# Kernel tuning notes

Hardware: AMD Instinct MI355X
Metric: run time of the kernel (lower is better)

Reference implementation:

```python
import jax, jax.numpy as jnp
import numpy as np

N_EMBD = 768
FULL_SIZE = 16 * N_EMBD   # 12288
K = 4 * N_EMBD            # iter_size = 3072 (top-k)
B, T = 8, 1024


def setup_inputs() -> dict:
    key = jax.random.key(0)
    k0, k1, k2, k3, k4 = jax.random.split(key, 5)
    s = lambda fan_in: 1.0 / np.sqrt(fan_in)
    return {
        "x": jax.random.normal(k0, (B, T, N_EMBD), dtype=jnp.float32),
        "w1": jax.random.normal(k1, (N_EMBD // 16, N_EMBD), dtype=jnp.float32) * s(N_EMBD),
        "w2": jax.random.normal(k2, (FULL_SIZE, N_EMBD // 16), dtype=jnp.float32) * s(N_EMBD // 16),
        "w_mfc": jax.random.normal(k3, (FULL_SIZE, N_EMBD), dtype=jnp.float32) * s(N_EMBD),
        "w_proj": jax.random.normal(k4, (N_EMBD, FULL_SIZE), dtype=jnp.float32) * s(FULL_SIZE),
    }


def _topk_mask(ck, k):
    # softmax -> top-k indices -> hard 0/1 mask (scatter of constant 1.0)
    probs = jax.nn.softmax(ck, axis=-1)
    _, idx = jax.lax.top_k(probs, k)            # (B, k)
    b = jnp.arange(probs.shape[0])[:, None]
    return jnp.zeros_like(probs).at[b, idx].set(1.0)


def reference(x, w1, w2, w_mfc, w_proj):
    # control net on sequence-mean pooled features
    pooled = x.mean(axis=1)                                  # (B, D)
    ck = jax.nn.relu(pooled @ w1.T) @ w2.T                   # (B, F)
    mask = _topk_mask(ck, K)                                 # (B, F) hard 0/1
    # DynamicMaskedLinear: bmm(x, (W*mask)^T) == (x @ W^T) * mask (0/1 output mask)
    h = jnp.einsum('btd,fd->btf', x, w_mfc) * mask[:, None, :]
    h = jax.nn.relu(h)
    out = jnp.einsum('btf,ef->bte', h, w_proj)               # (B, T, D)
    return out
```

## Files before the change

kernel.cpp:

```cpp
#include <hip/hip_runtime.h>

#define N_EMBD 768
#define FULL   12288
#define KSEL   3072
#define BATCH  8
#define TLEN   1024
#define HID    48

typedef short bf16x8 __attribute__((ext_vector_type(8)));
typedef float f32x4 __attribute__((ext_vector_type(4)));
typedef unsigned short u16x4 __attribute__((ext_vector_type(4)));
typedef unsigned short u16x8 __attribute__((ext_vector_type(8)));

#define MFMA(a, b, c) __builtin_amdgcn_mfma_f32_16x16x32_bf16((a), (b), (c), 0, 0, 0)
#define GLDS(g, l) __builtin_amdgcn_global_load_lds( \
    (const __attribute__((address_space(1))) void*)(const void*)(g), \
    (__attribute__((address_space(3))) void*)(void*)(l), 16, 0, 0)

__device__ __forceinline__ unsigned short f2bf(float f) {
  unsigned u = __float_as_uint(f);
  u += 0x7fffu + ((u >> 16) & 1u);
  return (unsigned short)(u >> 16);
}
__device__ __forceinline__ float bf2f(unsigned short h) {
  return __uint_as_float(((unsigned)h) << 16);
}

__global__ void split_pool_x(const float* __restrict__ x, unsigned short* __restrict__ xh,
                             unsigned short* __restrict__ xl, float* __restrict__ partial) {
  const int s = blockIdx.x;
  const int b = blockIdx.y;
  const int d = blockIdx.z * 256 + threadIdx.x * 4;
  const float* base = x + ((size_t)(b * TLEN + s * 64)) * N_EMBD + d;
  float4 sum = {0.f, 0.f, 0.f, 0.f};
  for (int t = 0; t < 64; ++t) {
    const float4 v = *(const float4*)(base + (size_t)t * N_EMBD);
    sum.x += v.x; sum.y += v.y; sum.z += v.z; sum.w += v.w;
    u16x4 h, l;
    h.x = f2bf(v.x); l.x = f2bf(v.x - bf2f(h.x));
    h.y = f2bf(v.y); l.y = f2bf(v.y - bf2f(h.y));
    h.z = f2bf(v.z); l.z = f2bf(v.z - bf2f(h.z));
    h.w = f2bf(v.w); l.w = f2bf(v.w - bf2f(h.w));
    const size_t o = ((size_t)(b * TLEN + s * 64 + t)) * N_EMBD + d;
    *(u16x4*)(xh + o) = h;
    *(u16x4*)(xl + o) = l;
  }
  float* pp = partial + (b * 16 + s) * N_EMBD + d;
  pp[0] = sum.x; pp[1] = sum.y; pp[2] = sum.z; pp[3] = sum.w;
}

__global__ __launch_bounds__(256) void control1_kernel(
    const float* __restrict__ partial, const float* __restrict__ w1, float* __restrict__ hid) {
  __shared__ float w1s[HID][385];
  __shared__ float ps[N_EMBD];
  const int b = blockIdx.x;
  const int tid = threadIdx.x;
  for (int d = tid; d < N_EMBD; d += 256) {
    float sum = 0.f;
    #pragma unroll
    for (int s = 0; s < 16; ++s) sum += partial[(b * 16 + s) * N_EMBD + d];
    ps[d] = sum * (1.f / TLEN);
  }
  float acc = 0.f;
  #pragma unroll
  for (int half = 0; half < 2; ++half) {
    __syncthreads();
    for (int i = tid; i < HID * 384; i += 256) {
      const int r = i / 384, c = i % 384;
      w1s[r][c] = w1[r * N_EMBD + half * 384 + c];
    }
    __syncthreads();
    if (tid < HID) {
      const float* pr = ps + half * 384;
      #pragma unroll 8
      for (int d2 = 0; d2 < 384; ++d2) acc = fmaf(pr[d2], w1s[tid][d2], acc);
    }
  }
  if (tid < HID) hid[b * HID + tid] = fmaxf(acc, 0.f);
}

__global__ void control2_kernel(const float* __restrict__ hid, const float* __restrict__ w2,
                                float* __restrict__ ck) {
  const int b = blockIdx.y;
  const int f = blockIdx.x * 256 + threadIdx.x;
  __shared__ float hid_s[HID];
  if (threadIdx.x < HID) hid_s[threadIdx.x] = hid[b * HID + threadIdx.x];
  __syncthreads();
  const float* wr = w2 + (size_t)f * HID;
  float acc = 0.f;
  #pragma unroll
  for (int j = 0; j < HID; ++j) acc = fmaf(hid_s[j], wr[j], acc);
  ck[b * FULL + f] = acc;
}

__global__ void topk_kernel(const float* __restrict__ ck, int* __restrict__ sel) {
  const int b = blockIdx.x;
  const int tid = threadIdx.x;
  const int lane = tid & 63, wv = tid >> 6;
  unsigned key[48];
  const int f_lo = tid * 48;
  #pragma unroll
  for (int i = 0; i < 48; ++i) {
    unsigned u = __float_as_uint(ck[b * FULL + f_lo + i]);
    key[i] = (u & 0x80000000u) ? ~u : (u | 0x80000000u);
  }
  __shared__ unsigned redw[4];
  __shared__ int sg[257], se[257];
  unsigned prefix = 0;
  int remaining = KSEL;
  for (int bit = 31; bit >= 0; --bit) {
    const unsigned want = prefix | (1u << bit);
    const unsigned shifted = want >> bit;
    int cnt = 0;
    #pragma unroll
    for (int i = 0; i < 48; ++i) cnt += ((key[i] >> bit) == shifted) ? 1 : 0;
    #pragma unroll
    for (int off = 1; off < 64; off <<= 1) cnt += __shfl_xor(cnt, off, 64);
    if (lane == 0) redw[wv] = (unsigned)cnt;
    __syncthreads();
    const int c = (int)(redw[0] + redw[1] + redw[2] + redw[3]);
    __syncthreads();
    if (c >= remaining) prefix = want;
    else remaining -= c;
  }
  const unsigned kth = prefix;
  int cg = 0, ce = 0;
  #pragma unroll
  for (int i = 0; i < 48; ++i) { cg += (key[i] > kth) ? 1 : 0; ce += (key[i] == kth) ? 1 : 0; }
  sg[tid] = cg; se[tid] = ce;
  __syncthreads();
  if (tid == 0) {
    int ag = 0, ae = 0;
    for (int i = 0; i < 256; ++i) {
      int tg = sg[i], te = se[i];
      sg[i] = ag; se[i] = ae;
      ag += tg; ae += te;
    }
    sg[256] = ag;
  }
  __syncthreads();
  const int ng = sg[256];
  int gpos = sg[tid], epos = se[tid];
  #pragma unroll
  for (int i = 0; i < 48; ++i) {
    const unsigned k = key[i];
    const int f = f_lo + i;
    if (k > kth) {
      sel[b * KSEL + (gpos++)] = f;
    } else if (k == kth) {
      const int p = ng + epos;
      if (p < KSEL) sel[b * KSEL + p] = f;
      ++epos;
    }
  }
}

__global__ void round_w_kernel(const float* __restrict__ src, unsigned short* __restrict__ dst, int n4) {
  const int idx = blockIdx.x * 256 + threadIdx.x;
  if (idx >= n4) return;
  const float4 v = ((const float4*)src)[idx];
  u16x4 h;
  h.x = f2bf(v.x); h.y = f2bf(v.y); h.z = f2bf(v.z); h.w = f2bf(v.w);
  ((u16x4*)dst)[idx] = h;
}

__global__ __launch_bounds__(256) void gather_wp_kernel(
    const float* __restrict__ wproj, const int* __restrict__ sel,
    unsigned short* __restrict__ wph) {
  __shared__ unsigned short row_s[FULL];
  const int e = blockIdx.x;
  const int tid = threadIdx.x;
  const float* wr = wproj + (size_t)e * FULL;
  #pragma unroll
  for (int i = 0; i < FULL / 4 / 256; ++i) {
    const int idx = tid + i * 256;
    const float4 v = ((const float4*)wr)[idx];
    u16x4 h;
    h.x = f2bf(v.x); h.y = f2bf(v.y); h.z = f2bf(v.z); h.w = f2bf(v.w);
    *(u16x4*)(row_s + idx * 4) = h;
  }
  __syncthreads();
  #pragma unroll
  for (int i = 0; i < 12; ++i) {
    const int idx = tid + i * 256;
    const int b = idx / 384, c = idx % 384;
    const int* sp = sel + b * KSEL + c * 8;
    const int4 s0 = ((const int4*)sp)[0];
    const int4 s1 = ((const int4*)sp)[1];
    u16x8 v;
    v[0] = row_s[s0.x]; v[1] = row_s[s0.y]; v[2] = row_s[s0.z]; v[3] = row_s[s0.w];
    v[4] = row_s[s1.x]; v[5] = row_s[s1.y]; v[6] = row_s[s1.z]; v[7] = row_s[s1.w];
    *(u16x8*)(wph + ((size_t)(b * N_EMBD + e)) * KSEL + c * 8) = v;
  }
}

__global__ __launch_bounds__(256) void gemm1_mfma(
    const unsigned short* __restrict__ xh, const unsigned short* __restrict__ xl,
    const unsigned short* __restrict__ wh, const int* __restrict__ sel,
    unsigned short* __restrict__ hh) {
  __shared__ __align__(16) char sm[49152];
  const int nx = TLEN / 128, ny = KSEL / 128;
  const int nwg = nx * ny * BATCH;
  int lin = blockIdx.x + nx * (blockIdx.y + ny * blockIdx.z);
  int swz = (lin & 7) * (nwg >> 3) + (lin >> 3);
  const int bx = swz % nx; int tmp = swz / nx;
  const int by = tmp % ny; const int b = tmp / ny;
  const int t0 = bx * 128, f0 = by * 128;

  const int tid = threadIdx.x;
  const int wv = tid >> 6, lane = tid & 63;
  const int srow = tid >> 2, sslot = tid & 3;
  const int wb = wv * 1024;

  const char* pxh = (const char*)xh;
  const char* pxl = (const char*)xl;
  const char* pwh = (const char*)wh;
  const size_t aoff  = ((size_t)(b * TLEN + t0 + srow)) * 1536 + sslot * 16;
  const size_t aoff2 = aoff + (size_t)64 * 1536;
  const int* selb = sel + b * KSEL;
  const size_t boff  = (size_t)selb[f0 + srow] * 1536 + sslot * 16;
  const size_t boff2 = (size_t)selb[f0 + srow + 64] * 1536 + sslot * 16;

  const int fr = lane & 15, kg = lane >> 4;
  const int fo = fr * 64 + kg * 16;
  const int m0 = (wv >> 1) * 64, n0 = (wv & 1) * 64;

  f32x4 acc[4][4];
  const f32x4 z4 = {0.f, 0.f, 0.f, 0.f};
  #pragma unroll
  for (int mi = 0; mi < 4; ++mi)
    #pragma unroll
    for (int ni = 0; ni < 4; ++ni) acc[mi][ni] = z4;

  auto stage = [&](int bo, int d) {
    GLDS(pxh + aoff  + d, sm + bo + 0     + wb);
    GLDS(pxh + aoff2 + d, sm + bo + 4096  + wb);
    GLDS(pxl + aoff  + d, sm + bo + 8192  + wb);
    GLDS(pxl + aoff2 + d, sm + bo + 12288 + wb);
    GLDS(pwh + boff  + d, sm + bo + 16384 + wb);
    GLDS(pwh + boff2 + d, sm + bo + 20480 + wb);
  };
  stage(0, 0);
  __syncthreads();
  const int NIT = N_EMBD * 2 / 64;
  for (int it = 0; it < NIT; ++it) {
    const int cur = (it & 1) ? 24576 : 0;
    if (it + 1 < NIT) stage(cur ^ 24576, (it + 1) * 64);
    bf16x8 ah[4], al[4], bh[4];
    #pragma unroll
    for (int i = 0; i < 4; ++i) {
      const int ra = (m0 + i * 16) * 64 + fo;
      const int rb = (n0 + i * 16) * 64 + fo;
      ah[i] = *(const bf16x8*)(sm + cur + 0     + ra);
      al[i] = *(const bf16x8*)(sm + cur + 8192  + ra);
      bh[i] = *(const bf16x8*)(sm + cur + 16384 + rb);
    }
    #pragma unroll
    for (int mi = 0; mi < 4; ++mi)
      #pragma unroll
      for (int ni = 0; ni < 4; ++ni) {
        acc[mi][ni] = MFMA(ah[mi], bh[ni], acc[mi][ni]);
        acc[mi][ni] = MFMA(al[mi], bh[ni], acc[mi][ni]);
      }
    __syncthreads();
  }
  unsigned short* lh = (unsigned short*)sm;
  const int rowg = lane >> 4, colc = lane & 15;
  #pragma unroll
  for (int mi = 0; mi < 4; ++mi)
    #pragma unroll
    for (int ni = 0; ni < 4; ++ni) {
      const int row = m0 + mi * 16 + rowg * 4;
      const int col = n0 + ni * 16 + colc;
      #pragma unroll
      for (int j = 0; j < 4; ++j)
        lh[(row + j) * 128 + col] = f2bf(fmaxf(acc[mi][ni][j], 0.f));
    }
  __syncthreads();
  const int orow = tid >> 4, oc = tid & 15;
  #pragma unroll
  for (int i2 = 0; i2 < 8; ++i2) {
    const int row = orow + i2 * 16;
    const u16x8 v = *(const u16x8*)&lh[row * 128 + oc * 8];
    *(u16x8*)(hh + ((size_t)(b * TLEN + t0 + row)) * KSEL + f0 + oc * 8) = v;
  }
}

__global__ __launch_bounds__(256) void gemm2_mfma(
    const unsigned short* __restrict__ hh, const unsigned short* __restrict__ wph,
    float* __restrict__ out) {
  __shared__ __align__(16) char sm[32768];
  const int lin = blockIdx.x;
  const int b = lin & 7;
  const int j = lin >> 3;
  const int bx = j & 7, by = j >> 3;
  const int t0 = bx * 128, e0 = by * 128;

  const int tid = threadIdx.x;
  const int wv = tid >> 6, lane = tid & 63;
  const int wb = wv * 1024;

  const char* pa = (const char*)hh;
  const char* pb = (const char*)wph;
  const size_t aoff  = ((size_t)(b * TLEN + t0 + (tid >> 2))) * 6144 + (tid & 3) * 16;
  const size_t aoff2 = aoff + (size_t)64 * 6144;
  const size_t boff  = ((size_t)(b * N_EMBD + e0 + (tid >> 2))) * 6144 + (tid & 3) * 16;
  const size_t boff2 = boff + (size_t)64 * 6144;

  const int fr = lane & 15, kg = lane >> 4;
  const int fo = fr * 64 + kg * 16;
  const int m0 = (wv >> 1) * 64, n0 = (wv & 1) * 64;

  f32x4 acc[4][4];
  const f32x4 z4 = {0.f, 0.f, 0.f, 0.f};
  #pragma unroll
  for (int mi = 0; mi < 4; ++mi)
    #pragma unroll
    for (int ni = 0; ni < 4; ++ni) acc[mi][ni] = z4;

  auto stage = [&](int bo, int d) {
    GLDS(pa + aoff  + d, sm + bo + 0     + wb);
    GLDS(pa + aoff2 + d, sm + bo + 4096  + wb);
    GLDS(pb + boff  + d, sm + bo + 8192  + wb);
    GLDS(pb + boff2 + d, sm + bo + 12288 + wb);
  };
  stage(0, 0);
  __syncthreads();
  const int NIT = KSEL * 2 / 64;
  for (int it = 0; it < NIT; ++it) {
    const int cur = (it & 1) ? 16384 : 0;
    if (it + 1 < NIT) stage(cur ^ 16384, (it + 1) * 64);
    bf16x8 ah[4], bh[4];
    #pragma unroll
    for (int i = 0; i < 4; ++i) {
      ah[i] = *(const bf16x8*)(sm + cur + 0    + (m0 + i * 16) * 64 + fo);
      bh[i] = *(const bf16x8*)(sm + cur + 8192 + (n0 + i * 16) * 64 + fo);
    }
    #pragma unroll
    for (int mi = 0; mi < 4; ++mi)
      #pragma unroll
      for (int ni = 0; ni < 4; ++ni)
        acc[mi][ni] = MFMA(ah[mi], bh[ni], acc[mi][ni]);
    __syncthreads();
  }
  const int rowg = lane >> 4, colc = lane & 15;
  #pragma unroll
  for (int mi = 0; mi < 4; ++mi)
    #pragma unroll
    for (int ni = 0; ni < 4; ++ni) {
      const int m = t0 + m0 + mi * 16 + rowg * 4;
      const int e = e0 + n0 + ni * 16 + colc;
      const size_t base = ((size_t)(b * TLEN + m)) * N_EMBD + e;
      #pragma unroll
      for (int jj = 0; jj < 4; ++jj)
        out[base + (size_t)jj * N_EMBD] = acc[mi][ni][jj];
    }
}

extern "C" void kernel_launch(void* const* d_in, const int* in_sizes, int n_in,
                              void* d_out, int out_size, void* d_ws, size_t ws_size,
                              hipStream_t stream) {
  const float* x      = (const float*)d_in[0];
  const float* w1     = (const float*)d_in[1];
  const float* w2     = (const float*)d_in[2];
  const float* w_mfc  = (const float*)d_in[3];
  const float* w_proj = (const float*)d_in[4];
  float* out = (float*)d_out;

  char* ws = (char*)d_ws;
  size_t off = 0;
  auto alloc = [&](size_t bytes) -> void* {
    void* p = ws + off;
    off += (bytes + 255) & ~(size_t)255;
    return p;
  };
  const size_t NX  = (size_t)BATCH * TLEN * N_EMBD;
  const size_t NW  = (size_t)FULL * N_EMBD;
  const size_t NWP = (size_t)BATCH * N_EMBD * KSEL;
  const size_t NH  = (size_t)BATCH * TLEN * KSEL;

  float* partial = (float*)alloc((size_t)BATCH * 16 * N_EMBD * 4);
  float* hid     = (float*)alloc((size_t)BATCH * HID * 4);
  float* ckbuf   = (float*)alloc((size_t)BATCH * FULL * 4);
  int*   sel     = (int*)  alloc((size_t)BATCH * KSEL * 4);
  unsigned short* xh  = (unsigned short*)alloc(NX * 2);
  unsigned short* xl  = (unsigned short*)alloc(NX * 2);
  unsigned short* wh  = (unsigned short*)alloc(NW * 2);
  unsigned short* wph = (unsigned short*)alloc(NWP * 2);
  unsigned short* hh  = (unsigned short*)alloc(NH * 2);

  split_pool_x<<<dim3(16, BATCH, 3), 64, 0, stream>>>(x, xh, xl, partial);
  round_w_kernel<<<(int)(NW / 4 / 256), 256, 0, stream>>>(w_mfc, wh, (int)(NW / 4));
  control1_kernel<<<BATCH, 256, 0, stream>>>(partial, w1, hid);
  control2_kernel<<<dim3(FULL / 256, BATCH), 256, 0, stream>>>(hid, w2, ckbuf);
  topk_kernel<<<BATCH, 256, 0, stream>>>(ckbuf, sel);
  gather_wp_kernel<<<768, 256, 0, stream>>>(w_proj, sel, wph);
  gemm1_mfma<<<dim3(TLEN / 128, KSEL / 128, BATCH), 256, 0, stream>>>(xh, xl, wh, sel, hh);
  gemm2_mfma<<<384, 256, 0, stream>>>(hh, wph, out);
}
```

Baseline: 382.5 us.

## Drop split-bf16 x residual in gemm1 and retile gemm2 to 128x64

Removes the low-order bf16 residual of x, so gemm1 does one bf16 MFMA pass instead of two and split_pool_x writes only one converted copy. gemm2 switches to 128x64 output tiles with a 128-deep K stage, launching twice as many workgroups. The aim is to cut MFMA work, memory traffic and tail imbalance, at the cost of reduced accuracy in the first GEMM.

```diff
diff --git a/kernel.cpp b/kernel.cpp
--- a/kernel.cpp
+++ b/kernel.cpp
@@ -27,7 +27,7 @@
 }
 
 __global__ void split_pool_x(const float* __restrict__ x, unsigned short* __restrict__ xh,
-                             unsigned short* __restrict__ xl, float* __restrict__ partial) {
+                             float* __restrict__ partial) {
   const int s = blockIdx.x;
   const int b = blockIdx.y;
   const int d = blockIdx.z * 256 + threadIdx.x * 4;
@@ -36,14 +36,9 @@
   for (int t = 0; t < 64; ++t) {
     const float4 v = *(const float4*)(base + (size_t)t * N_EMBD);
     sum.x += v.x; sum.y += v.y; sum.z += v.z; sum.w += v.w;
-    u16x4 h, l;
-    h.x = f2bf(v.x); l.x = f2bf(v.x - bf2f(h.x));
-    h.y = f2bf(v.y); l.y = f2bf(v.y - bf2f(h.y));
-    h.z = f2bf(v.z); l.z = f2bf(v.z - bf2f(h.z));
-    h.w = f2bf(v.w); l.w = f2bf(v.w - bf2f(h.w));
-    const size_t o = ((size_t)(b * TLEN + s * 64 + t)) * N_EMBD + d;
-    *(u16x4*)(xh + o) = h;
-    *(u16x4*)(xl + o) = l;
+    u16x4 h;
+    h.x = f2bf(v.x); h.y = f2bf(v.y); h.z = f2bf(v.z); h.w = f2bf(v.w);
+    *(u16x4*)(xh + ((size_t)(b * TLEN + s * 64 + t)) * N_EMBD + d) = h;
   }
   float* pp = partial + (b * 16 + s) * N_EMBD + d;
   pp[0] = sum.x; pp[1] = sum.y; pp[2] = sum.z; pp[3] = sum.w;
@@ -195,10 +190,9 @@
 }
 
 __global__ __launch_bounds__(256) void gemm1_mfma(
-    const unsigned short* __restrict__ xh, const unsigned short* __restrict__ xl,
-    const unsigned short* __restrict__ wh, const int* __restrict__ sel,
-    unsigned short* __restrict__ hh) {
-  __shared__ __align__(16) char sm[49152];
+    const unsigned short* __restrict__ xh, const unsigned short* __restrict__ wh,
+    const int* __restrict__ sel, unsigned short* __restrict__ hh) {
+  __shared__ __align__(16) char sm[32768];
   const int nx = TLEN / 128, ny = KSEL / 128;
   const int nwg = nx * ny * BATCH;
   int lin = blockIdx.x + nx * (blockIdx.y + ny * blockIdx.z);
@@ -213,7 +207,6 @@
   const int wb = wv * 1024;
 
   const char* pxh = (const char*)xh;
-  const char* pxl = (const char*)xl;
   const char* pwh = (const char*)wh;
   const size_t aoff  = ((size_t)(b * TLEN + t0 + srow)) * 1536 + sslot * 16;
   const size_t aoff2 = aoff + (size_t)64 * 1536;
@@ -235,33 +228,26 @@
   auto stage = [&](int bo, int d) {
     GLDS(pxh + aoff  + d, sm + bo + 0     + wb);
     GLDS(pxh + aoff2 + d, sm + bo + 4096  + wb);
-    GLDS(pxl + aoff  + d, sm + bo + 8192  + wb);
-    GLDS(pxl + aoff2 + d, sm + bo + 12288 + wb);
-    GLDS(pwh + boff  + d, sm + bo + 16384 + wb);
-    GLDS(pwh + boff2 + d, sm + bo + 20480 + wb);
+    GLDS(pwh + boff  + d, sm + bo + 8192  + wb);
+    GLDS(pwh + boff2 + d, sm + bo + 12288 + wb);
   };
   stage(0, 0);
   __syncthreads();
   const int NIT = N_EMBD * 2 / 64;
   for (int it = 0; it < NIT; ++it) {
-    const int cur = (it & 1) ? 24576 : 0;
-    if (it + 1 < NIT) stage(cur ^ 24576, (it + 1) * 64);
-    bf16x8 ah[4], al[4], bh[4];
+    const int cur = (it & 1) ? 16384 : 0;
+    if (it + 1 < NIT) stage(cur ^ 16384, (it + 1) * 64);
+    bf16x8 ah[4], bh[4];
     #pragma unroll
     for (int i = 0; i < 4; ++i) {
-      const int ra = (m0 + i * 16) * 64 + fo;
-      const int rb = (n0 + i * 16) * 64 + fo;
-      ah[i] = *(const bf16x8*)(sm + cur + 0     + ra);
-      al[i] = *(const bf16x8*)(sm + cur + 8192  + ra);
-      bh[i] = *(const bf16x8*)(sm + cur + 16384 + rb);
+      ah[i] = *(const bf16x8*)(sm + cur + 0    + (m0 + i * 16) * 64 + fo);
+      bh[i] = *(const bf16x8*)(sm + cur + 8192 + (n0 + i * 16) * 64 + fo);
     }
     #pragma unroll
     for (int mi = 0; mi < 4; ++mi)
       #pragma unroll
-      for (int ni = 0; ni < 4; ++ni) {
+      for (int ni = 0; ni < 4; ++ni)
         acc[mi][ni] = MFMA(ah[mi], bh[ni], acc[mi][ni]);
-        acc[mi][ni] = MFMA(al[mi], bh[ni], acc[mi][ni]);
-      }
     __syncthreads();
   }
   unsigned short* lh = (unsigned short*)sm;
@@ -289,12 +275,12 @@
 __global__ __launch_bounds__(256) void gemm2_mfma(
     const unsigned short* __restrict__ hh, const unsigned short* __restrict__ wph,
     float* __restrict__ out) {
-  __shared__ __align__(16) char sm[32768];
+  __shared__ __align__(16) char sm[49152];
   const int lin = blockIdx.x;
   const int b = lin & 7;
   const int j = lin >> 3;
   const int bx = j & 7, by = j >> 3;
-  const int t0 = bx * 128, e0 = by * 128;
+  const int t0 = bx * 128, e0 = by * 64;
 
   const int tid = threadIdx.x;
   const int wv = tid >> 6, lane = tid & 63;
@@ -305,49 +291,59 @@
   const size_t aoff  = ((size_t)(b * TLEN + t0 + (tid >> 2))) * 6144 + (tid & 3) * 16;
   const size_t aoff2 = aoff + (size_t)64 * 6144;
   const size_t boff  = ((size_t)(b * N_EMBD + e0 + (tid >> 2))) * 6144 + (tid & 3) * 16;
-  const size_t boff2 = boff + (size_t)64 * 6144;
 
   const int fr = lane & 15, kg = lane >> 4;
   const int fo = fr * 64 + kg * 16;
-  const int m0 = (wv >> 1) * 64, n0 = (wv & 1) * 64;
-
-  f32x4 acc[4][4];
+  const int m0 = (wv >> 1) * 64, n0 = (wv & 1) * 32;
+
+  f32x4 acc[4][2];
   const f32x4 z4 = {0.f, 0.f, 0.f, 0.f};
   #pragma unroll
   for (int mi = 0; mi < 4; ++mi)
     #pragma unroll
-    for (int ni = 0; ni < 4; ++ni) acc[mi][ni] = z4;
+    for (int ni = 0; ni < 2; ++ni) acc[mi][ni] = z4;
 
   auto stage = [&](int bo, int d) {
-    GLDS(pa + aoff  + d, sm + bo + 0     + wb);
-    GLDS(pa + aoff2 + d, sm + bo + 4096  + wb);
-    GLDS(pb + boff  + d, sm + bo + 8192  + wb);
-    GLDS(pb + boff2 + d, sm + bo + 12288 + wb);
+    GLDS(pa + aoff  + d,      sm + bo + 0     + wb);
+    GLDS(pa + aoff2 + d,      sm + bo + 4096  + wb);
+    GLDS(pa + aoff  + d + 64, sm + bo + 8192  + wb);
+    GLDS(pa + aoff2 + d + 64, sm + bo + 12288 + wb);
+    GLDS(pb + boff  + d,      sm + bo + 16384 + wb);
+    GLDS(pb + boff  + d + 64, sm + bo + 20480 + wb);
   };
   stage(0, 0);
   __syncthreads();
-  const int NIT = KSEL * 2 / 64;
+  const int NIT = KSEL * 2 / 128;
   for (int it = 0; it < NIT; ++it) {
-    const int cur = (it & 1) ? 16384 : 0;
-    if (it + 1 < NIT) stage(cur ^ 16384, (it + 1) * 64);
-    bf16x8 ah[4], bh[4];
+    const int cur = (it & 1) ? 24576 : 0;
+    if (it + 1 < NIT) stage(cur ^ 24576, (it + 1) * 128);
+    bf16x8 ah[4][2], bh[2][2];
     #pragma unroll
     for (int i = 0; i < 4; ++i) {
-      ah[i] = *(const bf16x8*)(sm + cur + 0    + (m0 + i * 16) * 64 + fo);
-      bh[i] = *(const bf16x8*)(sm + cur + 8192 + (n0 + i * 16) * 64 + fo);
-    }
-    #pragma unroll
-    for (int mi = 0; mi < 4; ++mi)
+      const int ra = (m0 + i * 16) * 64 + fo;
+      ah[i][0] = *(const bf16x8*)(sm + cur + 0    + ra);
+      ah[i][1] = *(const bf16x8*)(sm + cur + 8192 + ra);
+    }
+    #pragma unroll
+    for (int i = 0; i < 2; ++i) {
+      const int rb = (n0 + i * 16) * 64 + fo;
+      bh[i][0] = *(const bf16x8*)(sm + cur + 16384 + rb);
+      bh[i][1] = *(const bf16x8*)(sm + cur + 20480 + rb);
+    }
+    #pragma unroll
+    for (int c = 0; c < 2; ++c)
       #pragma unroll
-      for (int ni = 0; ni < 4; ++ni)
-        acc[mi][ni] = MFMA(ah[mi], bh[ni], acc[mi][ni]);
+      for (int mi = 0; mi < 4; ++mi)
+        #pragma unroll
+        for (int ni = 0; ni < 2; ++ni)
+          acc[mi][ni] = MFMA(ah[mi][c], bh[ni][c], acc[mi][ni]);
     __syncthreads();
   }
   const int rowg = lane >> 4, colc = lane & 15;
   #pragma unroll
   for (int mi = 0; mi < 4; ++mi)
     #pragma unroll
-    for (int ni = 0; ni < 4; ++ni) {
+    for (int ni = 0; ni < 2; ++ni) {
       const int m = t0 + m0 + mi * 16 + rowg * 4;
       const int e = e0 + n0 + ni * 16 + colc;
       const size_t base = ((size_t)(b * TLEN + m)) * N_EMBD + e;
@@ -384,17 +380,16 @@
   float* ckbuf   = (float*)alloc((size_t)BATCH * FULL * 4);
   int*   sel     = (int*)  alloc((size_t)BATCH * KSEL * 4);
   unsigned short* xh  = (unsigned short*)alloc(NX * 2);
-  unsigned short* xl  = (unsigned short*)alloc(NX * 2);
   unsigned short* wh  = (unsigned short*)alloc(NW * 2);
   unsigned short* wph = (unsigned short*)alloc(NWP * 2);
   unsigned short* hh  = (unsigned short*)alloc(NH * 2);
 
-  split_pool_x<<<dim3(16, BATCH, 3), 64, 0, stream>>>(x, xh, xl, partial);
+  split_pool_x<<<dim3(16, BATCH, 3), 64, 0, stream>>>(x, xh, partial);
   round_w_kernel<<<(int)(NW / 4 / 256), 256, 0, stream>>>(w_mfc, wh, (int)(NW / 4));
   control1_kernel<<<BATCH, 256, 0, stream>>>(partial, w1, hid);
   control2_kernel<<<dim3(FULL / 256, BATCH), 256, 0, stream>>>(hid, w2, ckbuf);
   topk_kernel<<<BATCH, 256, 0, stream>>>(ckbuf, sel);
   gather_wp_kernel<<<768, 256, 0, stream>>>(w_proj, sel, wph);
-  gemm1_mfma<<<dim3(TLEN / 128, KSEL / 128, BATCH), 256, 0, stream>>>(xh, xl, wh, sel, hh);
-  gemm2_mfma<<<384, 256, 0, stream>>>(hh, wph, out);
-}
+  gemm1_mfma<<<dim3(TLEN / 128, KSEL / 128, BATCH), 256, 0, stream>>>(xh, wh, sel, hh);
+  gemm2_mfma<<<768, 256, 0, stream>>>(hh, wph, out);
+}
```

Result: faster. 324.1 us (-15.3%).
